# Kernel tuning notes

Measured on AMD Instinct MI355X. Metric: run time of the kernel, lower is better.

Reference implementation:

```python
import jax, jax.numpy as jnp
import numpy as np

B, S, D, H = 2, 2048, 1024, 16
DK = D // H


def setup_inputs() -> dict:
    key = jax.random.key(0)
    ks = jax.random.split(key, 8)
    xavier = lambda k, shape: jax.random.uniform(k, shape, jnp.float32, -1.0, 1.0) * np.sqrt(6.0 / (shape[0] + shape[1]))
    return {
        "query": jax.random.normal(ks[0], (B, S, D), jnp.float32),
        "key": jax.random.normal(ks[1], (B, S, D), jnp.float32),
        "value": jax.random.normal(ks[2], (B, S, D), jnp.float32),
        # causal mask: True above the diagonal -> masked out
        "mask": jnp.broadcast_to(jnp.triu(jnp.ones((S, S), bool), k=1), (B, S, S)),
        "w_q": xavier(ks[3], (D, D)),  # torch Linear weight [out, in]
        "w_k": xavier(ks[4], (D, D)),
        "w_v": xavier(ks[5], (D, D)),
        "w_o": xavier(ks[6], (D, D)),
        "b_o": jnp.zeros((D,), jnp.float32),
    }


def reference(query, key, value, mask, w_q, w_k, w_v, w_o, b_o):
    b, sq, d = query.shape
    sk = key.shape[1]
    # projections (torch Linear: x @ W.T)
    Q = (query @ w_q.T).reshape(b, sq, H, DK).transpose(0, 2, 1, 3)  # [B,H,Sq,DK]
    K = (key @ w_k.T).reshape(b, sk, H, DK).transpose(0, 2, 1, 3)
    V = (value @ w_v.T).reshape(b, sk, H, DK).transpose(0, 2, 1, 3)
    scores = jnp.einsum('bhqd,bhkd->bhqk', Q, K) / np.sqrt(DK)
    scores = jnp.where(mask[:, None, :, :], jnp.float32(-1e9), scores)
    attn = jax.nn.softmax(scores, axis=-1)  # dropout is identity in eval
    out = jnp.einsum('bhqk,bhkd->bhqd', attn, V)
    out = out.transpose(0, 2, 1, 3).reshape(b, sq, d)
    return out @ w_o.T + b_o
```

## Files before the change

kernel.cpp:

```cpp
#include <hip/hip_runtime.h>
#include <hip/hip_bf16.h>
#include <stdint.h>


typedef __attribute__((ext_vector_type(4))) float  f32x4;
typedef __attribute__((ext_vector_type(4))) int    i32x4;
typedef __attribute__((ext_vector_type(8))) __bf16 bf16x8;
typedef __attribute__((ext_vector_type(4))) __bf16 bf16x4;
typedef __attribute__((ext_vector_type(2))) __bf16 bf16x2;

#define MFMA16(a, b, c) __builtin_amdgcn_mfma_f32_16x16x32_bf16((a), (b), (c), 0, 0, 0)

__device__ __forceinline__ void async16(const void* g, void* lds) {
  __builtin_amdgcn_global_load_lds(
      (const __attribute__((address_space(1))) uint32_t*)g,
      (__attribute__((address_space(3))) uint32_t*)lds,
      16, 0, 0);
}

__device__ __forceinline__ bf16x8 lds_swz_read(const __bf16* base, int row, int cchunk) {
  const int sw = cchunk ^ (row & 7);
  return *(const bf16x8*)((const char*)base + row * 128 + sw * 16);
}

__global__ void detect_dtype(const uint16_t* __restrict__ w, int* __restrict__ flag) {
  __shared__ int s;
  if (threadIdx.x == 0) s = 0;
  __syncthreads();
  int big = 0;
  for (int i = threadIdx.x; i < 8192; i += 256) {
    uint32_t u = ((uint32_t)w[i]) << 16;
    float f;
    __builtin_memcpy(&f, &u, 4);
    if (fabsf(f) > 1.0f) big = 1;
  }
  if (big) atomicOr(&s, 1);
  __syncthreads();
  if (threadIdx.x == 0) *flag = s;
}

struct CvtArgs { const void* src[8]; void* dst[8]; int n[8]; };

__global__ __launch_bounds__(256)
void convert_all(CvtArgs a, const int* __restrict__ flagp) {
  if (*flagp == 0) return;
  const int t = blockIdx.y;
  const int n = a.n[t];
  const int i0 = (blockIdx.x * 256 + threadIdx.x) * 8;
  if (i0 >= n) return;
  const float* s = (const float*)a.src[t];
  __bf16* d = (__bf16*)a.dst[t];
  bf16x8 v;
#pragma unroll
  for (int j = 0; j < 8; ++j) v[j] = (__bf16)s[i0 + j];
  *(bf16x8*)(d + i0) = v;
}

struct GemmArgs {
  const __bf16* A[3];    const __bf16* W[3];
  const __bf16* Acvt[3]; const __bf16* Wcvt[3];
  void* C[3]; float scale[3];
  const __bf16* bias; const __bf16* biascvt;
  const int* flagp; int mode;
};

__global__ __launch_bounds__(256, 3)
void gemm_nt(GemmArgs ga)
{
  constexpr int K = 1024;
  __shared__ __align__(16) __bf16 smem[16384];

  const int id = blockIdx.x + (blockIdx.y << 3) + (blockIdx.z << 8);
  const int mb = (id & 7) * 4 + ((id >> 3) & 3);
  const int rest = id >> 5;
  const int nb = rest & 7;
  const int z = rest >> 3;

  const int f = *ga.flagp;
  const __bf16* __restrict__ A = f ? ga.Acvt[z] : ga.A[z];
  const __bf16* __restrict__ W = f ? ga.Wcvt[z] : ga.W[z];
  void* __restrict__ C = ga.C[z];
  const float scale = ga.scale[z];
  const int mode = ga.mode;

  const int tid = threadIdx.x;
  const int lane = tid & 63;
  const int wave = tid >> 6;
  const int l15 = lane & 15;
  const int quad = lane >> 4;
  const int bm = mb * 128;
  const int bn = nb * 128;
  const int wm = (wave >> 1) * 64;
  const int wn = (wave & 1) * 64;

  auto stage = [&](int kt, int buf) {
    const int k0 = kt * 32;
    __bf16* As = smem + buf * 8192;
    __bf16* Bs = As + 4096;
#pragma unroll
    for (int r = 0; r < 2; ++r) {
      const int chunk = r * 256 + wave * 64 + lane;
      const int row = chunk >> 2, c = chunk & 3;
      async16(A + (size_t)(bm + row) * K + k0 + c * 8, As + (r * 256 + wave * 64) * 8);
      async16(W + (size_t)(bn + row) * K + k0 + c * 8, Bs + (r * 256 + wave * 64) * 8);
    }
  };

  f32x4 acc[4][4];
#pragma unroll
  for (int mi = 0; mi < 4; ++mi)
#pragma unroll
    for (int ni = 0; ni < 4; ++ni) {
      f32x4 zz = {0.f, 0.f, 0.f, 0.f};
      acc[mi][ni] = zz;
    }

  stage(0, 0);
  __syncthreads();

  for (int kt = 0; kt < K / 32; ++kt) {
    const int cur = kt & 1;
    const __bf16* As = smem + cur * 8192;
    const __bf16* Bs = As + 4096;

    bf16x8 af[4];
    bf16x8 bfr[4];
#pragma unroll
    for (int mi = 0; mi < 4; ++mi)
      af[mi] = *(const bf16x8*)(As + (wm + mi * 16 + l15) * 32 + quad * 8);
#pragma unroll
    for (int ni = 0; ni < 4; ++ni)
      bfr[ni] = *(const bf16x8*)(Bs + (wn + ni * 16 + l15) * 32 + quad * 8);

    if (kt + 1 < K / 32) stage(kt + 1, cur ^ 1);

#pragma unroll
    for (int mi = 0; mi < 4; ++mi)
#pragma unroll
      for (int ni = 0; ni < 4; ++ni)
        acc[mi][ni] = MFMA16(af[mi], bfr[ni], acc[mi][ni]);

    __syncthreads();
  }

  float bv[4] = {0.f, 0.f, 0.f, 0.f};
  if (mode == 1) {
    const __bf16* bias = f ? ga.biascvt : ga.bias;
#pragma unroll
    for (int ni = 0; ni < 4; ++ni) bv[ni] = (float)bias[bn + wn + ni * 16 + l15];
  }
  __bf16 (*Cs)[136] = (__bf16(*)[136])smem;

#pragma unroll
  for (int pass = 0; pass < 2; ++pass) {
    __syncthreads();
    if ((wave >> 1) == pass) {
#pragma unroll
      for (int mi = 0; mi < 4; ++mi)
#pragma unroll
        for (int ni = 0; ni < 4; ++ni)
#pragma unroll
          for (int r = 0; r < 4; ++r)
            Cs[mi * 16 + quad * 4 + r][wn + ni * 16 + l15] =
                (__bf16)(acc[mi][ni][r] * scale + bv[ni]);
    }
    __syncthreads();

    if (mode == 0) {
#pragma unroll
      for (int it = 0; it < 4; ++it) {
        const int cid = it * 256 + tid;
        const int off = cid & 7, seg = cid >> 3;
        const int hl = seg & 1, rowl = seg >> 1;
        f32x4 v = *(const f32x4*)(&Cs[rowl][hl * 64 + off * 8]);
        const int m = bm + pass * 64 + rowl;
        const int b = m >> 11, s = m & 2047;
        const int h = (bn >> 6) + hl;
        *(f32x4*)((__bf16*)C + ((size_t)(b * 16 + h) * 2048 + s) * 64 + off * 8) = v;
      }
    } else if (f) {
#pragma unroll
      for (int it = 0; it < 4; ++it) {
        const int cid = it * 256 + tid;
        const int off = cid & 15, rowl = cid >> 4;
        bf16x8 vb = *(const bf16x8*)(&Cs[rowl][off * 8]);
        const int m = bm + pass * 64 + rowl;
        float* dst = (float*)C + (size_t)m * 1024 + bn + off * 8;
        f32x4 lo, hi;
#pragma unroll
        for (int j = 0; j < 4; ++j) { lo[j] = (float)vb[j]; hi[j] = (float)vb[4 + j]; }
        *(f32x4*)dst = lo;
        *(f32x4*)(dst + 4) = hi;
      }
    } else {
#pragma unroll
      for (int it = 0; it < 4; ++it) {
        const int cid = it * 256 + tid;
        const int off = cid & 15, rowl = cid >> 4;
        bf16x8 vb = *(const bf16x8*)(&Cs[rowl][off * 8]);
        const int m = bm + pass * 64 + rowl;
        *(bf16x8*)((__bf16*)C + (size_t)m * 1024 + bn + off * 8) = vb;
      }
    }
  }
}

__global__ __launch_bounds__(256, 3)
void attn(const __bf16* __restrict__ Q,
          const __bf16* __restrict__ Kg,
          const __bf16* __restrict__ Vg,
          __bf16* __restrict__ O)
{
  __shared__ __align__(16) __bf16 Ks[2][128 * 64];
  __shared__ __align__(16) __bf16 Vts[64][136];

  const int tid = threadIdx.x;
  const int lane = tid & 63;
  const int wave = tid >> 6;
  const int l15 = lane & 15;
  const int quad = lane >> 4;

  const int zb = blockIdx.x;
  const int qt = 31 - (zb >> 5);
  const int bh = zb & 31;
  const int q0 = qt * 64;
  const int nIter = (qt >> 1) + 1;

  const __bf16* Qp = Q + (size_t)bh * 2048 * 64;
  const __bf16* Kp = Kg + (size_t)bh * 2048 * 64;
  const __bf16* Vp = Vg + (size_t)bh * 2048 * 64;

  const int qrow_wl = wave * 16 + l15;

  bf16x8 qf[2];
#pragma unroll
  for (int kc = 0; kc < 2; ++kc)
    qf[kc] = *(const bf16x8*)(Qp + (size_t)(q0 + qrow_wl) * 64 + kc * 32 + quad * 8);

  f32x4 o_[4];
#pragma unroll
  for (int dt = 0; dt < 4; ++dt) {
    f32x4 zz = {0.f, 0.f, 0.f, 0.f};
    o_[dt] = zz;
  }
  float lsum = 0.0f;

  const int pp4 = tid & 31;
  const int dgg = tid >> 5;
  const int P0 = (((pp4 & 0x18) | ((pp4 & 3) << 1) | ((pp4 >> 2) & 1)) << 2);

#pragma unroll
  for (int r = 0; r < 4; ++r) {
    const int chunk = r * 256 + tid;
    const int row = chunk >> 3, c = (chunk & 7) ^ (row & 7);
    async16(Kp + (size_t)row * 64 + c * 8,
            (char*)&Ks[0][0] + (r * 256 + wave * 64) * 16);
  }
  bf16x8 va0 = *(const bf16x8*)(Vp + (size_t)(4 * pp4 + 0) * 64 + dgg * 8);
  bf16x8 va1 = *(const bf16x8*)(Vp + (size_t)(4 * pp4 + 1) * 64 + dgg * 8);
  bf16x8 va2 = *(const bf16x8*)(Vp + (size_t)(4 * pp4 + 2) * 64 + dgg * 8);
  bf16x8 va3 = *(const bf16x8*)(Vp + (size_t)(4 * pp4 + 3) * 64 + dgg * 8);

  for (int t = 0; t < nIter; ++t) {
    const int cur = t & 1;

#pragma unroll
    for (int j = 0; j < 8; ++j) {
      bf16x4 w = { va0[j], va1[j], va2[j], va3[j] };
      *(bf16x4*)(&Vts[dgg * 8 + j][P0]) = w;
    }
    __syncthreads();

    bf16x8 vn0 = va0, vn1 = va1, vn2 = va2, vn3 = va3;
    if (t + 1 < nIter) {
      const int k1 = (t + 1) * 128;
#pragma unroll
      for (int r = 0; r < 4; ++r) {
        const int chunk = r * 256 + tid;
        const int row = chunk >> 3, c = (chunk & 7) ^ (row & 7);
        async16(Kp + (size_t)(k1 + row) * 64 + c * 8,
                (char*)&Ks[cur ^ 1][0] + (r * 256 + wave * 64) * 16);
      }
      vn0 = *(const bf16x8*)(Vp + (size_t)(k1 + 4 * pp4 + 0) * 64 + dgg * 8);
      vn1 = *(const bf16x8*)(Vp + (size_t)(k1 + 4 * pp4 + 1) * 64 + dgg * 8);
      vn2 = *(const bf16x8*)(Vp + (size_t)(k1 + 4 * pp4 + 2) * 64 + dgg * 8);
      vn3 = *(const bf16x8*)(Vp + (size_t)(k1 + 4 * pp4 + 3) * 64 + dgg * 8);
    }

    f32x4 st[8];
#pragma unroll
    for (int nt = 0; nt < 8; ++nt) {
      f32x4 zz = {0.f, 0.f, 0.f, 0.f};
      st[nt] = zz;
    }
    __builtin_amdgcn_s_setprio(1);
#pragma unroll
    for (int kc = 0; kc < 2; ++kc)
#pragma unroll
      for (int nt = 0; nt < 8; ++nt) {
        bf16x8 kf = lds_swz_read(&Ks[cur][0], nt * 16 + l15, kc * 4 + quad);
        st[nt] = MFMA16(kf, qf[kc], st[nt]);
      }
    __builtin_amdgcn_s_setprio(0);

    if (t == (qt >> 1)) {
      const int k0 = t * 128;
#pragma unroll
      for (int nt = 0; nt < 8; ++nt)
#pragma unroll
        for (int r = 0; r < 4; ++r)
          if (k0 + nt * 16 + quad * 4 + r > q0 + qrow_wl) st[nt][r] = -1e30f;
    }

    bf16x8 pf[4];
#pragma unroll
    for (int nt = 0; nt < 8; ++nt)
#pragma unroll
      for (int r = 0; r < 4; ++r) {
        const float pv = __builtin_amdgcn_exp2f(st[nt][r]);
        lsum += pv;
        pf[nt >> 1][(nt & 1) * 4 + r] = (__bf16)pv;
      }

    __builtin_amdgcn_s_setprio(1);
#pragma unroll
    for (int kc = 0; kc < 4; ++kc)
#pragma unroll
      for (int dt = 0; dt < 4; ++dt) {
        bf16x8 vf = *(const bf16x8*)(&Vts[dt * 16 + l15][kc * 32 + quad * 8]);
        o_[dt] = MFMA16(vf, pf[kc], o_[dt]);
      }
    __builtin_amdgcn_s_setprio(0);

    __syncthreads();
    va0 = vn0; va1 = vn1; va2 = vn2; va3 = vn3;
  }

  lsum += __shfl_xor(lsum, 16, 64);
  lsum += __shfl_xor(lsum, 32, 64);

  __bf16 (*Ot)[72] = (__bf16(*)[72])&Vts[0][0];
  const float inv_l = 1.0f / lsum;
#pragma unroll
  for (int dt = 0; dt < 4; ++dt)
#pragma unroll
    for (int r = 0; r < 4; r += 2) {
      bf16x2 pr = { (__bf16)(o_[dt][r] * inv_l),
                    (__bf16)(o_[dt][r + 1] * inv_l) };
      *(bf16x2*)(&Ot[qrow_wl][dt * 16 + quad * 4 + r]) = pr;
    }
  __syncthreads();

  const int b = bh >> 4, h = bh & 15;
#pragma unroll
  for (int t = 0; t < 2; ++t) {
    const int i = t * 256 + tid;
    const int row = i >> 3, c = i & 7;
    f32x4 v = *(const f32x4*)(&Ot[row][c * 8]);
    *(f32x4*)(O + (size_t)(b * 2048 + q0 + row) * 1024 + h * 64 + c * 8) = v;
  }
}

extern "C" void kernel_launch(void* const* d_in, const int* in_sizes, int n_in,
                              void* d_out, int out_size, void* d_ws, size_t ws_size,
                              hipStream_t stream) {
  char* ws = (char*)d_ws;
  int* flag = (int*)ws;
  __bf16* Xc0 = (__bf16*)(ws + (1u << 20));
  __bf16* Xc1 = (__bf16*)(ws + (9u << 20));
  __bf16* Xc2 = (__bf16*)(ws + (17u << 20));
  __bf16* Wc0 = (__bf16*)(ws + (25u << 20));
  __bf16* Wc1 = (__bf16*)(ws + (27u << 20));
  __bf16* Wc2 = (__bf16*)(ws + (29u << 20));
  __bf16* Wc3 = (__bf16*)(ws + (31u << 20));
  __bf16* bc  = (__bf16*)(ws + (33u << 20));
  __bf16* Qw  = (__bf16*)(ws + (34u << 20));
  __bf16* Kw  = (__bf16*)(ws + (42u << 20));
  __bf16* Vw  = (__bf16*)(ws + (50u << 20));
  __bf16* Aw  = (__bf16*)(ws + (58u << 20));

  detect_dtype<<<1, 256, 0, stream>>>((const uint16_t*)d_in[4], flag);

  CvtArgs ca;
  ca.src[0] = d_in[0]; ca.dst[0] = Xc0; ca.n[0] = 4194304;
  ca.src[1] = d_in[1]; ca.dst[1] = Xc1; ca.n[1] = 4194304;
  ca.src[2] = d_in[2]; ca.dst[2] = Xc2; ca.n[2] = 4194304;
  ca.src[3] = d_in[4]; ca.dst[3] = Wc0; ca.n[3] = 1048576;
  ca.src[4] = d_in[5]; ca.dst[4] = Wc1; ca.n[4] = 1048576;
  ca.src[5] = d_in[6]; ca.dst[5] = Wc2; ca.n[5] = 1048576;
  ca.src[6] = d_in[7]; ca.dst[6] = Wc3; ca.n[6] = 1048576;
  ca.src[7] = d_in[8]; ca.dst[7] = bc;  ca.n[7] = 1024;
  convert_all<<<dim3(2048, 8), 256, 0, stream>>>(ca, flag);

  GemmArgs g0;
  g0.A[0] = (const __bf16*)d_in[0]; g0.Acvt[0] = Xc0;
  g0.A[1] = (const __bf16*)d_in[1]; g0.Acvt[1] = Xc1;
  g0.A[2] = (const __bf16*)d_in[2]; g0.Acvt[2] = Xc2;
  g0.W[0] = (const __bf16*)d_in[4]; g0.Wcvt[0] = Wc0;
  g0.W[1] = (const __bf16*)d_in[5]; g0.Wcvt[1] = Wc1;
  g0.W[2] = (const __bf16*)d_in[6]; g0.Wcvt[2] = Wc2;
  g0.C[0] = Qw; g0.scale[0] = 0.18033688f;
  g0.C[1] = Kw; g0.scale[1] = 1.0f;
  g0.C[2] = Vw; g0.scale[2] = 1.0f;
  g0.bias = nullptr; g0.biascvt = nullptr; g0.flagp = flag; g0.mode = 0;
  gemm_nt<<<dim3(8, 32, 3), 256, 0, stream>>>(g0);

  attn<<<dim3(1024), 256, 0, stream>>>(Qw, Kw, Vw, Aw);

  GemmArgs g1;
  g1.A[0] = Aw; g1.Acvt[0] = Aw;
  g1.A[1] = nullptr; g1.Acvt[1] = nullptr;
  g1.A[2] = nullptr; g1.Acvt[2] = nullptr;
  g1.W[0] = (const __bf16*)d_in[7]; g1.Wcvt[0] = Wc3;
  g1.W[1] = nullptr; g1.Wcvt[1] = nullptr;
  g1.W[2] = nullptr; g1.Wcvt[2] = nullptr;
  g1.C[0] = d_out; g1.scale[0] = 1.0f;
  g1.C[1] = nullptr; g1.scale[1] = 0.f;
  g1.C[2] = nullptr; g1.scale[2] = 0.f;
  g1.bias = (const __bf16*)d_in[8]; g1.biascvt = bc;
  g1.flagp = flag; g1.mode = 1;
  gemm_nt<<<dim3(8, 32, 1), 256, 0, stream>>>(g1);
}
```

Measured before the change: 229.8 us.

## Single-buffer K tile through registers to raise attention occupancy

The attention kernel stops double-buffering K in LDS with async global-to-LDS loads. It now prefetches the next K tile into registers and writes it to one LDS buffer at the top of each iteration, the same way V is already handled. This cuts LDS use per block, and launch bounds go from 3 to 4 blocks per CU to exploit that. In exchange it adds register pressure, extra VGPR-to-LDS store instructions, and loses the asynchronous load path.

```diff
diff --git a/kernel.cpp b/kernel.cpp
--- a/kernel.cpp
+++ b/kernel.cpp
@@ -205,13 +205,13 @@
   }
 }
 
-__global__ __launch_bounds__(256, 3)
+__global__ __launch_bounds__(256, 4)
 void attn(const __bf16* __restrict__ Q,
           const __bf16* __restrict__ Kg,
           const __bf16* __restrict__ Vg,
           __bf16* __restrict__ O)
 {
-  __shared__ __align__(16) __bf16 Ks[2][128 * 64];
+  __shared__ __align__(16) __bf16 Ks[128 * 64];
   __shared__ __align__(16) __bf16 Vts[64][136];
 
   const int tid = threadIdx.x;
@@ -245,25 +245,31 @@
   }
   float lsum = 0.0f;
 
+  const int krow[4] = { (0 * 256 + tid) >> 3, (1 * 256 + tid) >> 3,
+                        (2 * 256 + tid) >> 3, (3 * 256 + tid) >> 3 };
+  const int kcol[4] = { ((0 * 256 + tid) & 7) ^ (krow[0] & 7),
+                        ((1 * 256 + tid) & 7) ^ (krow[1] & 7),
+                        ((2 * 256 + tid) & 7) ^ (krow[2] & 7),
+                        ((3 * 256 + tid) & 7) ^ (krow[3] & 7) };
+
   const int pp4 = tid & 31;
   const int dgg = tid >> 5;
   const int P0 = (((pp4 & 0x18) | ((pp4 & 3) << 1) | ((pp4 >> 2) & 1)) << 2);
 
-#pragma unroll
-  for (int r = 0; r < 4; ++r) {
-    const int chunk = r * 256 + tid;
-    const int row = chunk >> 3, c = (chunk & 7) ^ (row & 7);
-    async16(Kp + (size_t)row * 64 + c * 8,
-            (char*)&Ks[0][0] + (r * 256 + wave * 64) * 16);
-  }
+  bf16x8 ka0 = *(const bf16x8*)(Kp + (size_t)krow[0] * 64 + kcol[0] * 8);
+  bf16x8 ka1 = *(const bf16x8*)(Kp + (size_t)krow[1] * 64 + kcol[1] * 8);
+  bf16x8 ka2 = *(const bf16x8*)(Kp + (size_t)krow[2] * 64 + kcol[2] * 8);
+  bf16x8 ka3 = *(const bf16x8*)(Kp + (size_t)krow[3] * 64 + kcol[3] * 8);
   bf16x8 va0 = *(const bf16x8*)(Vp + (size_t)(4 * pp4 + 0) * 64 + dgg * 8);
   bf16x8 va1 = *(const bf16x8*)(Vp + (size_t)(4 * pp4 + 1) * 64 + dgg * 8);
   bf16x8 va2 = *(const bf16x8*)(Vp + (size_t)(4 * pp4 + 2) * 64 + dgg * 8);
   bf16x8 va3 = *(const bf16x8*)(Vp + (size_t)(4 * pp4 + 3) * 64 + dgg * 8);
 
   for (int t = 0; t < nIter; ++t) {
-    const int cur = t & 1;
-
+    *(bf16x8*)((char*)Ks + (0 * 256 + tid) * 16) = ka0;
+    *(bf16x8*)((char*)Ks + (1 * 256 + tid) * 16) = ka1;
+    *(bf16x8*)((char*)Ks + (2 * 256 + tid) * 16) = ka2;
+    *(bf16x8*)((char*)Ks + (3 * 256 + tid) * 16) = ka3;
 #pragma unroll
     for (int j = 0; j < 8; ++j) {
       bf16x4 w = { va0[j], va1[j], va2[j], va3[j] };
@@ -271,16 +277,14 @@
     }
     __syncthreads();
 
+    bf16x8 kn0 = ka0, kn1 = ka1, kn2 = ka2, kn3 = ka3;
     bf16x8 vn0 = va0, vn1 = va1, vn2 = va2, vn3 = va3;
     if (t + 1 < nIter) {
       const int k1 = (t + 1) * 128;
-#pragma unroll
-      for (int r = 0; r < 4; ++r) {
-        const int chunk = r * 256 + tid;
-        const int row = chunk >> 3, c = (chunk & 7) ^ (row & 7);
-        async16(Kp + (size_t)(k1 + row) * 64 + c * 8,
-                (char*)&Ks[cur ^ 1][0] + (r * 256 + wave * 64) * 16);
-      }
+      kn0 = *(const bf16x8*)(Kp + (size_t)(k1 + krow[0]) * 64 + kcol[0] * 8);
+      kn1 = *(const bf16x8*)(Kp + (size_t)(k1 + krow[1]) * 64 + kcol[1] * 8);
+      kn2 = *(const bf16x8*)(Kp + (size_t)(k1 + krow[2]) * 64 + kcol[2] * 8);
+      kn3 = *(const bf16x8*)(Kp + (size_t)(k1 + krow[3]) * 64 + kcol[3] * 8);
       vn0 = *(const bf16x8*)(Vp + (size_t)(k1 + 4 * pp4 + 0) * 64 + dgg * 8);
       vn1 = *(const bf16x8*)(Vp + (size_t)(k1 + 4 * pp4 + 1) * 64 + dgg * 8);
       vn2 = *(const bf16x8*)(Vp + (size_t)(k1 + 4 * pp4 + 2) * 64 + dgg * 8);
@@ -298,7 +302,7 @@
     for (int kc = 0; kc < 2; ++kc)
 #pragma unroll
       for (int nt = 0; nt < 8; ++nt) {
-        bf16x8 kf = lds_swz_read(&Ks[cur][0], nt * 16 + l15, kc * 4 + quad);
+        bf16x8 kf = lds_swz_read(Ks, nt * 16 + l15, kc * 4 + quad);
         st[nt] = MFMA16(kf, qf[kc], st[nt]);
       }
     __builtin_amdgcn_s_setprio(0);
@@ -333,6 +337,7 @@
     __builtin_amdgcn_s_setprio(0);
 
     __syncthreads();
+    ka0 = kn0; ka1 = kn1; ka2 = kn2; ka3 = kn3;
     va0 = vn0; va1 = vn1; va2 = vn2; va3 = vn3;
   }
 
```

Result: no change. 233.0 us (+1.4%).

## Fuse fp32-to-bf16 activation conversion into QKV projection GEMM loads

Applied to the files above, without the earlier changes.

The separate pass that converts the three fp32 activation tensors to bf16 is removed. The QKV GEMM now loads fp32 A tiles straight into registers, converts them, and writes bf16 into LDS after the MFMAs, while weights still stream through async LDS loads. This removes a full read/write round trip of about 48MB of activations, but register-staged loads replace async-to-LDS copies for A and raise register pressure in the GEMM mainloop.

```diff
diff --git a/kernel.cpp b/kernel.cpp
--- a/kernel.cpp
+++ b/kernel.cpp
@@ -4,7 +4,6 @@
 
 
 typedef __attribute__((ext_vector_type(4))) float  f32x4;
-typedef __attribute__((ext_vector_type(4))) int    i32x4;
 typedef __attribute__((ext_vector_type(8))) __bf16 bf16x8;
 typedef __attribute__((ext_vector_type(4))) __bf16 bf16x4;
 typedef __attribute__((ext_vector_type(2))) __bf16 bf16x2;
@@ -39,7 +38,7 @@
   if (threadIdx.x == 0) *flag = s;
 }
 
-struct CvtArgs { const void* src[8]; void* dst[8]; int n[8]; };
+struct CvtArgs { const void* src[5]; void* dst[5]; int n[5]; };
 
 __global__ __launch_bounds__(256)
 void convert_all(CvtArgs a, const int* __restrict__ flagp) {
@@ -61,13 +60,14 @@
   const __bf16* Acvt[3]; const __bf16* Wcvt[3];
   void* C[3]; float scale[3];
   const __bf16* bias; const __bf16* biascvt;
-  const int* flagp; int mode;
+  const int* flagp; int mode; int aCvt;
 };
 
 __global__ __launch_bounds__(256, 3)
 void gemm_nt(GemmArgs ga)
 {
   constexpr int K = 1024;
+  constexpr int NT = K / 32;
   __shared__ __align__(16) __bf16 smem[16384];
 
   const int id = blockIdx.x + (blockIdx.y << 3) + (blockIdx.z << 8);
@@ -77,8 +77,10 @@
   const int z = rest >> 3;
 
   const int f = *ga.flagp;
-  const __bf16* __restrict__ A = f ? ga.Acvt[z] : ga.A[z];
-  const __bf16* __restrict__ W = f ? ga.Wcvt[z] : ga.W[z];
+  const int aF32 = ga.aCvt & f;
+  const float*  __restrict__ Af = (const float*)ga.A[z];
+  const __bf16* __restrict__ A  = f ? ga.Acvt[z] : ga.A[z];
+  const __bf16* __restrict__ W  = f ? ga.Wcvt[z] : ga.W[z];
   void* __restrict__ C = ga.C[z];
   const float scale = ga.scale[z];
   const int mode = ga.mode;
@@ -93,15 +95,26 @@
   const int wm = (wave >> 1) * 64;
   const int wn = (wave & 1) * 64;
 
-  auto stage = [&](int kt, int buf) {
+  const int row0 = (0 * 256 + tid) >> 2, c0 = (0 * 256 + tid) & 3;
+  const int row1 = (1 * 256 + tid) >> 2, c1 = (1 * 256 + tid) & 3;
+
+  auto stageA16 = [&](int kt, int buf) {
     const int k0 = kt * 32;
     __bf16* As = smem + buf * 8192;
-    __bf16* Bs = As + 4096;
 #pragma unroll
     for (int r = 0; r < 2; ++r) {
       const int chunk = r * 256 + wave * 64 + lane;
       const int row = chunk >> 2, c = chunk & 3;
       async16(A + (size_t)(bm + row) * K + k0 + c * 8, As + (r * 256 + wave * 64) * 8);
+    }
+  };
+  auto stageW16 = [&](int kt, int buf) {
+    const int k0 = kt * 32;
+    __bf16* Bs = smem + buf * 8192 + 4096;
+#pragma unroll
+    for (int r = 0; r < 2; ++r) {
+      const int chunk = r * 256 + wave * 64 + lane;
+      const int row = chunk >> 2, c = chunk & 3;
       async16(W + (size_t)(bn + row) * K + k0 + c * 8, Bs + (r * 256 + wave * 64) * 8);
     }
   };
@@ -115,10 +128,27 @@
       acc[mi][ni] = zz;
     }
 
-  stage(0, 0);
+  if (aF32) {
+    f32x4 a0 = *(const f32x4*)(Af + (size_t)(bm + row0) * K + c0 * 8);
+    f32x4 a1 = *(const f32x4*)(Af + (size_t)(bm + row0) * K + c0 * 8 + 4);
+    f32x4 a2 = *(const f32x4*)(Af + (size_t)(bm + row1) * K + c1 * 8);
+    f32x4 a3 = *(const f32x4*)(Af + (size_t)(bm + row1) * K + c1 * 8 + 4);
+    bf16x8 v0, v1;
+#pragma unroll
+    for (int j = 0; j < 4; ++j) {
+      v0[j] = (__bf16)a0[j]; v0[4 + j] = (__bf16)a1[j];
+      v1[j] = (__bf16)a2[j]; v1[4 + j] = (__bf16)a3[j];
+    }
+    *(bf16x8*)(smem + (0 * 256 + tid) * 8) = v0;
+    *(bf16x8*)(smem + (1 * 256 + tid) * 8) = v1;
+    stageW16(0, 0);
+  } else {
+    stageA16(0, 0);
+    stageW16(0, 0);
+  }
   __syncthreads();
 
-  for (int kt = 0; kt < K / 32; ++kt) {
+  for (int kt = 0; kt < NT; ++kt) {
     const int cur = kt & 1;
     const __bf16* As = smem + cur * 8192;
     const __bf16* Bs = As + 4096;
@@ -132,13 +162,38 @@
     for (int ni = 0; ni < 4; ++ni)
       bfr[ni] = *(const bf16x8*)(Bs + (wn + ni * 16 + l15) * 32 + quad * 8);
 
-    if (kt + 1 < K / 32) stage(kt + 1, cur ^ 1);
+    f32x4 pa0, pa1, pa2, pa3;
+    const int haveNext = (kt + 1 < NT);
+    if (haveNext) {
+      const int k1 = (kt + 1) * 32;
+      if (aF32) {
+        pa0 = *(const f32x4*)(Af + (size_t)(bm + row0) * K + k1 + c0 * 8);
+        pa1 = *(const f32x4*)(Af + (size_t)(bm + row0) * K + k1 + c0 * 8 + 4);
+        pa2 = *(const f32x4*)(Af + (size_t)(bm + row1) * K + k1 + c1 * 8);
+        pa3 = *(const f32x4*)(Af + (size_t)(bm + row1) * K + k1 + c1 * 8 + 4);
+      } else {
+        stageA16(kt + 1, cur ^ 1);
+      }
+      stageW16(kt + 1, cur ^ 1);
+    }
 
 #pragma unroll
     for (int mi = 0; mi < 4; ++mi)
 #pragma unroll
       for (int ni = 0; ni < 4; ++ni)
         acc[mi][ni] = MFMA16(af[mi], bfr[ni], acc[mi][ni]);
+
+    if (haveNext && aF32) {
+      __bf16* Ad = smem + (cur ^ 1) * 8192;
+      bf16x8 v0, v1;
+#pragma unroll
+      for (int j = 0; j < 4; ++j) {
+        v0[j] = (__bf16)pa0[j]; v0[4 + j] = (__bf16)pa1[j];
+        v1[j] = (__bf16)pa2[j]; v1[4 + j] = (__bf16)pa3[j];
+      }
+      *(bf16x8*)(Ad + (0 * 256 + tid) * 8) = v0;
+      *(bf16x8*)(Ad + (1 * 256 + tid) * 8) = v1;
+    }
 
     __syncthreads();
   }
@@ -366,9 +421,6 @@
                               hipStream_t stream) {
   char* ws = (char*)d_ws;
   int* flag = (int*)ws;
-  __bf16* Xc0 = (__bf16*)(ws + (1u << 20));
-  __bf16* Xc1 = (__bf16*)(ws + (9u << 20));
-  __bf16* Xc2 = (__bf16*)(ws + (17u << 20));
   __bf16* Wc0 = (__bf16*)(ws + (25u << 20));
   __bf16* Wc1 = (__bf16*)(ws + (27u << 20));
   __bf16* Wc2 = (__bf16*)(ws + (29u << 20));
@@ -382,20 +434,17 @@
   detect_dtype<<<1, 256, 0, stream>>>((const uint16_t*)d_in[4], flag);
 
   CvtArgs ca;
-  ca.src[0] = d_in[0]; ca.dst[0] = Xc0; ca.n[0] = 4194304;
-  ca.src[1] = d_in[1]; ca.dst[1] = Xc1; ca.n[1] = 4194304;
-  ca.src[2] = d_in[2]; ca.dst[2] = Xc2; ca.n[2] = 4194304;
-  ca.src[3] = d_in[4]; ca.dst[3] = Wc0; ca.n[3] = 1048576;
-  ca.src[4] = d_in[5]; ca.dst[4] = Wc1; ca.n[4] = 1048576;
-  ca.src[5] = d_in[6]; ca.dst[5] = Wc2; ca.n[5] = 1048576;
-  ca.src[6] = d_in[7]; ca.dst[6] = Wc3; ca.n[6] = 1048576;
-  ca.src[7] = d_in[8]; ca.dst[7] = bc;  ca.n[7] = 1024;
-  convert_all<<<dim3(2048, 8), 256, 0, stream>>>(ca, flag);
+  ca.src[0] = d_in[4]; ca.dst[0] = Wc0; ca.n[0] = 1048576;
+  ca.src[1] = d_in[5]; ca.dst[1] = Wc1; ca.n[1] = 1048576;
+  ca.src[2] = d_in[6]; ca.dst[2] = Wc2; ca.n[2] = 1048576;
+  ca.src[3] = d_in[7]; ca.dst[3] = Wc3; ca.n[3] = 1048576;
+  ca.src[4] = d_in[8]; ca.dst[4] = bc;  ca.n[4] = 1024;
+  convert_all<<<dim3(512, 5), 256, 0, stream>>>(ca, flag);
 
   GemmArgs g0;
-  g0.A[0] = (const __bf16*)d_in[0]; g0.Acvt[0] = Xc0;
-  g0.A[1] = (const __bf16*)d_in[1]; g0.Acvt[1] = Xc1;
-  g0.A[2] = (const __bf16*)d_in[2]; g0.Acvt[2] = Xc2;
+  g0.A[0] = (const __bf16*)d_in[0]; g0.Acvt[0] = (const __bf16*)d_in[0];
+  g0.A[1] = (const __bf16*)d_in[1]; g0.Acvt[1] = (const __bf16*)d_in[1];
+  g0.A[2] = (const __bf16*)d_in[2]; g0.Acvt[2] = (const __bf16*)d_in[2];
   g0.W[0] = (const __bf16*)d_in[4]; g0.Wcvt[0] = Wc0;
   g0.W[1] = (const __bf16*)d_in[5]; g0.Wcvt[1] = Wc1;
   g0.W[2] = (const __bf16*)d_in[6]; g0.Wcvt[2] = Wc2;
@@ -403,6 +452,7 @@
   g0.C[1] = Kw; g0.scale[1] = 1.0f;
   g0.C[2] = Vw; g0.scale[2] = 1.0f;
   g0.bias = nullptr; g0.biascvt = nullptr; g0.flagp = flag; g0.mode = 0;
+  g0.aCvt = 1;
   gemm_nt<<<dim3(8, 32, 3), 256, 0, stream>>>(g0);
 
   attn<<<dim3(1024), 256, 0, stream>>>(Qw, Kw, Vw, Aw);
@@ -418,6 +468,6 @@
   g1.C[1] = nullptr; g1.scale[1] = 0.f;
   g1.C[2] = nullptr; g1.scale[2] = 0.f;
   g1.bias = (const __bf16*)d_in[8]; g1.biascvt = bc;
-  g1.flagp = flag; g1.mode = 1;
+  g1.flagp = flag; g1.mode = 1; g1.aCvt = 0;
   gemm_nt<<<dim3(8, 32, 1), 256, 0, stream>>>(g1);
 }
```

Result: slower. 243.3 us (+5.9%).
